# Performance work log

Hardware: AMD Instinct MI355X
Metric: run time of the kernel (lower is better)

## Reference

```python
import jax, jax.numpy as jnp
import numpy as np

D_MODEL = 512
D_K = 64
D_V = 64
N_HEADS = 8
N = 4096
EPS = 1e-5


def setup_inputs() -> dict:
    key = jax.random.key(0)
    ks = jax.random.split(key, 12)
    s = 1.0 / np.sqrt(D_MODEL)
    return {
        "Q": jax.random.normal(ks[0], (N, D_MODEL), dtype=jnp.float32),
        "K": jax.random.normal(ks[1], (N, D_MODEL), dtype=jnp.float32),
        "V": jax.random.normal(ks[2], (N, D_MODEL), dtype=jnp.float32),
        "W_Q": jax.random.normal(ks[3], (D_K * N_HEADS, D_MODEL), dtype=jnp.float32) * s,
        "b_Q": jnp.zeros((D_K * N_HEADS,), jnp.float32),
        "W_K": jax.random.normal(ks[4], (D_K * N_HEADS, D_MODEL), dtype=jnp.float32) * s,
        "b_K": jnp.zeros((D_K * N_HEADS,), jnp.float32),
        "W_V": jax.random.normal(ks[5], (D_V * N_HEADS, D_MODEL), dtype=jnp.float32) * s,
        "b_V": jnp.zeros((D_V * N_HEADS,), jnp.float32),
        "W_O": jax.random.normal(ks[6], (D_MODEL, N_HEADS * D_V), dtype=jnp.float32) * s,
        "b_O": jnp.zeros((D_MODEL,), jnp.float32),
        "gamma": jnp.ones((D_MODEL,), jnp.float32),
        "beta": jnp.zeros((D_MODEL,), jnp.float32),
    }


def reference(Q, K, V, W_Q, b_Q, W_K, b_K, W_V, b_V, W_O, b_O, gamma, beta):
    n = Q.shape[0]
    # projections (torch Linear: x @ W.T + b), then split heads: [N, H, dk]
    Qs = (Q @ W_Q.T + b_Q).reshape(n, N_HEADS, D_K)
    Ks = (K @ W_K.T + b_K).reshape(n, N_HEADS, D_K)
    Vs = (V @ W_V.T + b_V).reshape(n, N_HEADS, D_V)
    # per-head scaled dot-product attention over the N dim, batched via einsum
    scores = jnp.einsum("nhd,mhd->hnm", Qs, Ks) / np.sqrt(D_K)  # [H, N, N]
    attn = jax.nn.softmax(scores, axis=-1)
    ctx = jnp.einsum("hnm,mhd->nhd", attn, Vs)  # [N, H, dv]
    context = ctx.reshape(n, N_HEADS * D_V)  # concat heads (matches torch.cat order)
    out = context @ W_O.T + b_O + Q  # output proj + residual
    # LayerNorm over last dim
    mu = jnp.mean(out, axis=-1, keepdims=True)
    var = jnp.mean((out - mu) ** 2, axis=-1, keepdims=True)
    return (out - mu) * jax.lax.rsqrt(var + EPS) * gamma + beta
```

## Files before the change

### kernel.cpp

```cpp
#include <hip/hip_runtime.h>
#include <cstdint>

#define N_TOK 4096
#define DMODEL 512
#define NHEADS 8
#define HDIM 64

typedef unsigned short u16;
typedef __bf16 bf16x8 __attribute__((ext_vector_type(8)));
typedef float f32x4 __attribute__((ext_vector_type(4)));

union U128 { uint4 u; bf16x8 b; u16 s[8]; };

__device__ __forceinline__ u16 f2bf(float f) {
  uint32_t u = __builtin_bit_cast(uint32_t, f);
  u += 0x7FFFu + ((u >> 16) & 1u);
  return (u16)(u >> 16);
}
__device__ __forceinline__ float bf2f(u16 s) {
  uint32_t u = ((uint32_t)s) << 16;
  return __builtin_bit_cast(float, u);
}
__device__ __forceinline__ uint32_t fbit(float f) { return __builtin_bit_cast(uint32_t, f); }

#if __has_builtin(__builtin_amdgcn_exp2f)
#define EXP2(x) __builtin_amdgcn_exp2f(x)
#else
#define EXP2(x) __expf((x) * 0.6931471805599453f)
#endif

__device__ __forceinline__ void ldg2lds16(const void* g, void* s) {
  __builtin_amdgcn_global_load_lds(
      (const __attribute__((address_space(1))) void*)g,
      (__attribute__((address_space(3))) void*)s, 16, 0, 0);
}

__global__ __launch_bounds__(256) void cvt7_kernel(
    const float* __restrict__ Q, const float* __restrict__ K, const float* __restrict__ V,
    const float* __restrict__ WQ, const float* __restrict__ WK, const float* __restrict__ WV,
    const float* __restrict__ WO,
    u16* __restrict__ Qb, u16* __restrict__ Kb, u16* __restrict__ Vb,
    u16* __restrict__ WQb, u16* __restrict__ WKb, u16* __restrict__ WVb,
    u16* __restrict__ WOb)
{
  int b = blockIdx.x;
  const float* src; u16* dst; int rel;
  if      (b < 2048) { src = Q;  dst = Qb;  rel = b; }
  else if (b < 4096) { src = K;  dst = Kb;  rel = b - 2048; }
  else if (b < 6144) { src = V;  dst = Vb;  rel = b - 4096; }
  else if (b < 6400) { src = WQ; dst = WQb; rel = b - 6144; }
  else if (b < 6656) { src = WK; dst = WKb; rel = b - 6400; }
  else if (b < 6912) { src = WV; dst = WVb; rel = b - 6656; }
  else               { src = WO; dst = WOb; rel = b - 6912; }
  int i = (rel * 256 + threadIdx.x) * 4;
  float4 f = *(const float4*)(src + i);
  ushort4 o;
  o.x = f2bf(f.x); o.y = f2bf(f.y); o.z = f2bf(f.z); o.w = f2bf(f.w);
  *(ushort4*)(dst + i) = o;
}

__global__ __launch_bounds__(256) void proj3_kernel(
    const u16* __restrict__ Qb, const u16* __restrict__ Kb, const u16* __restrict__ Vb,
    const u16* __restrict__ WQb, const u16* __restrict__ WKb, const u16* __restrict__ WVb,
    const float* __restrict__ bQ, const float* __restrict__ bK, const float* __restrict__ bV,
    u16* __restrict__ Qs, u16* __restrict__ Ks, u16* __restrict__ Vt)
{
  const int z = blockIdx.z;
  const u16* A      = (z == 0) ? Qb : (z == 1) ? Kb : Vb;
  const u16* W      = (z == 0) ? WQb : (z == 1) ? WKb : WVb;
  const float* bias = (z == 0) ? bQ : (z == 1) ? bK : bV;

  const int m0 = blockIdx.x * 128;
  const int j0 = blockIdx.y * 64;
  const int tid = threadIdx.x;
  const int w = tid >> 6, lane = tid & 63, quad = lane >> 4, l = lane & 15;

  __shared__ bf16x8 sA[2][8][128];
  __shared__ bf16x8 sB[2][8][64];

  const f32x4 zero = {0.f, 0.f, 0.f, 0.f};
  f32x4 acc[2][4];
#pragma unroll
  for (int m = 0; m < 2; ++m)
#pragma unroll
    for (int s = 0; s < 4; ++s) acc[m][s] = zero;

  auto stage = [&](int kt, int buf) {
    const int k0 = kt * 64;
#pragma unroll
    for (int i = 0; i < 4; ++i) {
      const int chunk = 2 * w + (i >> 1), half = (i & 1) * 64;
      const u16* ag = A + (size_t)(m0 + half + lane) * DMODEL + k0 + chunk * 8;
      ldg2lds16(ag, (char*)&sA[buf][chunk][half]);
    }
#pragma unroll
    for (int i = 0; i < 2; ++i) {
      const int chunk = 2 * w + i;
      const u16* bg = W + (size_t)(j0 + lane) * DMODEL + k0 + chunk * 8;
      ldg2lds16(bg, (char*)&sB[buf][chunk][0]);
    }
  };

  stage(0, 0);
  __syncthreads();
  for (int kt = 0; kt < 8; ++kt) {
    const int buf = kt & 1;
    if (kt + 1 < 8) stage(kt + 1, buf ^ 1);
#pragma unroll
    for (int c = 0; c < 2; ++c) {
      bf16x8 af0 = sA[buf][c * 4 + quad][w * 32 + l];
      bf16x8 af1 = sA[buf][c * 4 + quad][w * 32 + 16 + l];
#pragma unroll
      for (int s = 0; s < 4; ++s) {
        bf16x8 bfb = sB[buf][c * 4 + quad][s * 16 + l];
        acc[0][s] = __builtin_amdgcn_mfma_f32_16x16x32_bf16(af0, bfb, acc[0][s], 0, 0, 0);
        acc[1][s] = __builtin_amdgcn_mfma_f32_16x16x32_bf16(af1, bfb, acc[1][s], 0, 0, 0);
      }
    }
    __syncthreads();
  }

#pragma unroll
  for (int m = 0; m < 2; ++m)
#pragma unroll
    for (int s = 0; s < 4; ++s) {
      int j = j0 + s * 16 + l;
      float bv = bias[j];
      int n0 = m0 + w * 32 + m * 16 + quad * 4;
      if (z < 2) {
        u16* Y = (z == 0) ? Qs : Ks;
#pragma unroll
        for (int r = 0; r < 4; ++r)
          Y[(size_t)(n0 + r) * DMODEL + j] = f2bf(acc[m][s][r] + bv);
      } else {
        ushort4 pk;
        pk.x = f2bf(acc[m][s][0] + bv); pk.y = f2bf(acc[m][s][1] + bv);
        pk.z = f2bf(acc[m][s][2] + bv); pk.w = f2bf(acc[m][s][3] + bv);
        *(ushort4*)(Vt + (size_t)j * N_TOK + n0) = pk;
      }
    }
}

__global__ __launch_bounds__(512, 4) void attn_kernel(
    const u16* __restrict__ Qs, const u16* __restrict__ Ks,
    const u16* __restrict__ Vt, u16* __restrict__ Opart, float* __restrict__ Lpart)
{
  const int hs = blockIdx.x;
  const int h = hs & 7, split = hs >> 3;
  const int qt = blockIdx.y;
  const int tid = threadIdx.x;
  const int w = tid >> 6, lane = tid & 63, quad = lane >> 4, l = lane & 15;

  __shared__ bf16x8 kch[2][8][64];
  __shared__ bf16x8 vch[2][8][64];
  __shared__ __align__(16) u16 pbuf[8][32][40];

  const int wq0 = qt * 256 + w * 32;

  bf16x8 qf[2][2];
#pragma unroll
  for (int c = 0; c < 2; ++c)
#pragma unroll
    for (int m = 0; m < 2; ++m) {
      U128 u;
      u.u = *(const uint4*)(Qs + (size_t)(wq0 + m * 16 + l) * DMODEL + h * HDIM + c * 32 + quad * 8);
#pragma unroll
      for (int j = 0; j < 8; ++j) u.s[j] = f2bf(bf2f(u.s[j]) * 0.18033688f);
      qf[c][m] = u.b;
    }

  const f32x4 zero = {0.f, 0.f, 0.f, 0.f};
  f32x4 o[2][4];
  float lsum[2] = {0.f, 0.f};
#pragma unroll
  for (int m = 0; m < 2; ++m)
#pragma unroll
    for (int s = 0; s < 4; ++s) o[m][s] = zero;

  auto stage = [&](int it, int buf) {
    const int j0 = split * 1024 + it * 64;
    if (w < 4) {
      const u16* kg = Ks + (size_t)(j0 + lane) * DMODEL + h * HDIM + w * 16;
      ldg2lds16(kg,     (char*)&kch[buf][2 * w][0]);
      ldg2lds16(kg + 8, (char*)&kch[buf][2 * w + 1][0]);
    } else {
      const int w2 = w - 4;
      const u16* vg = Vt + (size_t)(h * HDIM + lane) * N_TOK + j0 + w2 * 16;
      ldg2lds16(vg,     (char*)&vch[buf][2 * w2][0]);
      ldg2lds16(vg + 8, (char*)&vch[buf][2 * w2 + 1][0]);
    }
  };

  stage(0, 0);
  __syncthreads();

  for (int it = 0; it < 16; ++it) {
    const int buf = it & 1;
    if (it + 1 < 16) stage(it + 1, buf ^ 1);

#pragma unroll
    for (int kh = 0; kh < 2; ++kh) {
#pragma unroll
      for (int tt = 0; tt < 2; ++tt) {
        const int t = kh * 2 + tt;
        f32x4 sacc[2];
        sacc[0] = zero; sacc[1] = zero;
#pragma unroll
        for (int c = 0; c < 2; ++c) {
          bf16x8 kf = kch[buf][c * 4 + quad][t * 16 + l];
          sacc[0] = __builtin_amdgcn_mfma_f32_16x16x32_bf16(kf, qf[c][0], sacc[0], 0, 0, 0);
          sacc[1] = __builtin_amdgcn_mfma_f32_16x16x32_bf16(kf, qf[c][1], sacc[1], 0, 0, 0);
        }
#pragma unroll
        for (int m = 0; m < 2; ++m) {
          float p0 = EXP2(sacc[m][0]);
          float p1 = EXP2(sacc[m][1]);
          float p2 = EXP2(sacc[m][2]);
          float p3 = EXP2(sacc[m][3]);
          lsum[m] += (p0 + p1) + (p2 + p3);
          uint2 st;
          st.x = (fbit(p0) >> 16) | (fbit(p1) & 0xFFFF0000u);
          st.y = (fbit(p2) >> 16) | (fbit(p3) & 0xFFFF0000u);
          *(uint2*)&pbuf[w][m * 16 + l][tt * 16 + quad * 4] = st;
        }
      }
      U128 pf0, pf1;
      pf0.u = *(const uint4*)&pbuf[w][l][quad * 8];
      pf1.u = *(const uint4*)&pbuf[w][16 + l][quad * 8];
#pragma unroll
      for (int s = 0; s < 4; ++s) {
        bf16x8 vf = vch[buf][kh * 4 + quad][s * 16 + l];
        o[0][s] = __builtin_amdgcn_mfma_f32_16x16x32_bf16(pf0.b, vf, o[0][s], 0, 0, 0);
        o[1][s] = __builtin_amdgcn_mfma_f32_16x16x32_bf16(pf1.b, vf, o[1][s], 0, 0, 0);
      }
    }
    __syncthreads();
  }

#pragma unroll
  for (int m = 0; m < 2; ++m) {
    lsum[m] += __shfl_xor(lsum[m], 16);
    lsum[m] += __shfl_xor(lsum[m], 32);
  }
  if (quad == 0) {
    Lpart[((size_t)split * NHEADS + h) * N_TOK + wq0 + l]      = lsum[0];
    Lpart[((size_t)split * NHEADS + h) * N_TOK + wq0 + 16 + l] = lsum[1];
  }
  u16* Ob = Opart + ((size_t)(split * NHEADS + h) * N_TOK + wq0) * 64;
#pragma unroll
  for (int m = 0; m < 2; ++m)
#pragma unroll
    for (int s = 0; s < 4; ++s)
#pragma unroll
      for (int r = 0; r < 4; ++r)
        Ob[(size_t)(m * 16 + quad * 4 + r) * 64 + s * 16 + l] = f2bf(o[m][s][r]);
}

__global__ __launch_bounds__(256) void combine_kernel(
    const u16* __restrict__ Opart, const float* __restrict__ Lpart,
    u16* __restrict__ ctx)
{
  int idx = blockIdx.x * 256 + threadIdx.x;
  int n = idx >> 6;
  int c8 = idx & 63;
  int h = c8 >> 3;
  int vd0 = (c8 & 7) * 8;

  float acc[8] = {0, 0, 0, 0, 0, 0, 0, 0};
  float lsum = 0.f;
#pragma unroll
  for (int s = 0; s < 4; ++s) {
    U128 u;
    u.u = *(const uint4*)(Opart + ((size_t)(s * NHEADS + h) * N_TOK + n) * 64 + vd0);
#pragma unroll
    for (int j = 0; j < 8; ++j) acc[j] += bf2f(u.s[j]);
    lsum += Lpart[((size_t)s * NHEADS + h) * N_TOK + n];
  }
  float inv = 1.f / lsum;
  U128 u;
#pragma unroll
  for (int j = 0; j < 8; ++j) u.s[j] = f2bf(acc[j] * inv);
  *(uint4*)(ctx + (size_t)n * DMODEL + h * HDIM + vd0) = u.u;
}

__global__ __launch_bounds__(256) void gemmo_kernel(
    const u16* __restrict__ ctx, const u16* __restrict__ WOb,
    const float* __restrict__ bO, const float* __restrict__ resid,
    float* __restrict__ Y)
{
  const int m0 = blockIdx.x * 128;
  const int j0 = blockIdx.y * 64;
  const int tid = threadIdx.x;
  const int w = tid >> 6, lane = tid & 63, quad = lane >> 4, l = lane & 15;

  __shared__ bf16x8 sA[2][8][128];
  __shared__ bf16x8 sB[2][8][64];

  const f32x4 zero = {0.f, 0.f, 0.f, 0.f};
  f32x4 acc[2][4];
#pragma unroll
  for (int m = 0; m < 2; ++m)
#pragma unroll
    for (int s = 0; s < 4; ++s) acc[m][s] = zero;

  auto stage = [&](int kt, int buf) {
    const int k0 = kt * 64;
#pragma unroll
    for (int i = 0; i < 4; ++i) {
      const int chunk = 2 * w + (i >> 1), half = (i & 1) * 64;
      const u16* ag = ctx + (size_t)(m0 + half + lane) * DMODEL + k0 + chunk * 8;
      ldg2lds16(ag, (char*)&sA[buf][chunk][half]);
    }
#pragma unroll
    for (int i = 0; i < 2; ++i) {
      const int chunk = 2 * w + i;
      const u16* bg = WOb + (size_t)(j0 + lane) * DMODEL + k0 + chunk * 8;
      ldg2lds16(bg, (char*)&sB[buf][chunk][0]);
    }
  };

  stage(0, 0);
  __syncthreads();
  for (int kt = 0; kt < 8; ++kt) {
    const int buf = kt & 1;
    if (kt + 1 < 8) stage(kt + 1, buf ^ 1);
#pragma unroll
    for (int c = 0; c < 2; ++c) {
      bf16x8 af0 = sA[buf][c * 4 + quad][w * 32 + l];
      bf16x8 af1 = sA[buf][c * 4 + quad][w * 32 + 16 + l];
#pragma unroll
      for (int s = 0; s < 4; ++s) {
        bf16x8 bfb = sB[buf][c * 4 + quad][s * 16 + l];
        acc[0][s] = __builtin_amdgcn_mfma_f32_16x16x32_bf16(af0, bfb, acc[0][s], 0, 0, 0);
        acc[1][s] = __builtin_amdgcn_mfma_f32_16x16x32_bf16(af1, bfb, acc[1][s], 0, 0, 0);
      }
    }
    __syncthreads();
  }
#pragma unroll
  for (int m = 0; m < 2; ++m)
#pragma unroll
    for (int s = 0; s < 4; ++s) {
      int j = j0 + s * 16 + l;
      float bv = bO[j];
      int n0 = m0 + w * 32 + m * 16 + quad * 4;
#pragma unroll
      for (int r = 0; r < 4; ++r)
        Y[(size_t)(n0 + r) * DMODEL + j] = acc[m][s][r] + bv + resid[(size_t)(n0 + r) * DMODEL + j];
    }
}

__global__ __launch_bounds__(256) void ln_kernel(
    const float* __restrict__ X, const float* __restrict__ gamma,
    const float* __restrict__ beta, float* __restrict__ Y)
{
  const int w = threadIdx.x >> 6, lane = threadIdx.x & 63;
  const int row = blockIdx.x * 4 + w;
  const float* x = X + (size_t)row * DMODEL + lane * 8;
  float4 a = *(const float4*)x;
  float4 b = *(const float4*)(x + 4);

  float s = a.x + a.y + a.z + a.w + b.x + b.y + b.z + b.w;
#pragma unroll
  for (int m = 1; m < 64; m <<= 1) s += __shfl_xor(s, m);
  float mu = s * (1.f / DMODEL);

  float d0 = a.x - mu, d1 = a.y - mu, d2 = a.z - mu, d3 = a.w - mu;
  float d4 = b.x - mu, d5 = b.y - mu, d6 = b.z - mu, d7 = b.w - mu;
  float v = d0*d0 + d1*d1 + d2*d2 + d3*d3 + d4*d4 + d5*d5 + d6*d6 + d7*d7;
#pragma unroll
  for (int m = 1; m < 64; m <<= 1) v += __shfl_xor(v, m);
  float sc = rsqrtf(v * (1.f / DMODEL) + 1e-5f);

  const float* g = gamma + lane * 8;
  const float* be = beta + lane * 8;
  float4 go = *(const float4*)g;
  float4 g1 = *(const float4*)(g + 4);
  float4 bo = *(const float4*)be;
  float4 b1 = *(const float4*)(be + 4);

  float4 y0, y1;
  y0.x = d0 * sc * go.x + bo.x;  y0.y = d1 * sc * go.y + bo.y;
  y0.z = d2 * sc * go.z + bo.z;  y0.w = d3 * sc * go.w + bo.w;
  y1.x = d4 * sc * g1.x + b1.x;  y1.y = d5 * sc * g1.y + b1.y;
  y1.z = d6 * sc * g1.z + b1.z;  y1.w = d7 * sc * g1.w + b1.w;

  float* yp = Y + (size_t)row * DMODEL + lane * 8;
  *(float4*)yp = y0;
  *(float4*)(yp + 4) = y1;
}

extern "C" void kernel_launch(void* const* d_in, const int* in_sizes, int n_in,
                              void* d_out, int out_size, void* d_ws, size_t ws_size,
                              hipStream_t stream)
{
  const float* Q     = (const float*)d_in[0];
  const float* K     = (const float*)d_in[1];
  const float* V     = (const float*)d_in[2];
  const float* WQ    = (const float*)d_in[3];
  const float* bQ    = (const float*)d_in[4];
  const float* WK    = (const float*)d_in[5];
  const float* bK    = (const float*)d_in[6];
  const float* WV    = (const float*)d_in[7];
  const float* bV    = (const float*)d_in[8];
  const float* WO    = (const float*)d_in[9];
  const float* bO    = (const float*)d_in[10];
  const float* gamma = (const float*)d_in[11];
  const float* beta  = (const float*)d_in[12];

  const size_t MB = 1ull << 20;
  char* ws = (char*)d_ws;
  u16* Qb   = (u16*)(ws + 0 * MB);
  u16* Kb   = (u16*)(ws + 4 * MB);
  u16* Vb   = (u16*)(ws + 8 * MB);
  u16* WQb  = (u16*)(ws + 12 * MB);
  u16* WKb  = (u16*)(ws + 12 * MB + 512 * 1024);
  u16* WVb  = (u16*)(ws + 13 * MB);
  u16* WOb  = (u16*)(ws + 13 * MB + 512 * 1024);
  u16* Qs   = (u16*)(ws + 14 * MB);
  u16* Ks   = (u16*)(ws + 18 * MB);
  u16* Vt   = (u16*)(ws + 22 * MB);
  u16* ctx  = (u16*)(ws + 26 * MB);
  u16* Opart = (u16*)(ws + 30 * MB);
  float* tmp = (float*)(ws + 30 * MB);
  float* Lpart = (float*)(ws + 46 * MB);
  float* out = (float*)d_out;

  cvt7_kernel<<<7168, 256, 0, stream>>>(Q, K, V, WQ, WK, WV, WO,
                                        Qb, Kb, Vb, WQb, WKb, WVb, WOb);
  proj3_kernel<<<dim3(32, 8, 3), 256, 0, stream>>>(Qb, Kb, Vb, WQb, WKb, WVb,
                                                   bQ, bK, bV, Qs, Ks, Vt);
  attn_kernel<<<dim3(32, 16), 512, 0, stream>>>(Qs, Ks, Vt, Opart, Lpart);
  combine_kernel<<<1024, 256, 0, stream>>>(Opart, Lpart, ctx);
  gemmo_kernel<<<dim3(32, 8), 256, 0, stream>>>(ctx, WOb, bO, Q, tmp);
  ln_kernel<<<1024, 256, 0, stream>>>(tmp, gamma, beta, out);
}
```

Before: 182.3 us.

## Widen attention per-wave query tile, double KV splits, shrink output-proj tile

The attention kernel now uses 4 waves per block, each holding 64 query rows instead of 32. Each K/V tile staged in LDS is therefore reused across more MFMAs per wave. The key range is split 8 ways instead of 4, so the grid doubles, and the combine kernel reduces over 8 partials. The output-projection GEMM tile is halved to 64 rows so more blocks launch. The trade-off is higher register pressure per attention wave and twice the partial-output traffic in the combine step.

```diff
diff --git a/kernel.cpp b/kernel.cpp
--- a/kernel.cpp
+++ b/kernel.cpp
@@ -141,7 +141,7 @@
     }
 }
 
-__global__ __launch_bounds__(512, 4) void attn_kernel(
+__global__ __launch_bounds__(256, 3) void attn_kernel(
     const u16* __restrict__ Qs, const u16* __restrict__ Ks,
     const u16* __restrict__ Vt, u16* __restrict__ Opart, float* __restrict__ Lpart)
 {
@@ -153,15 +153,15 @@
 
   __shared__ bf16x8 kch[2][8][64];
   __shared__ bf16x8 vch[2][8][64];
-  __shared__ __align__(16) u16 pbuf[8][32][40];
-
-  const int wq0 = qt * 256 + w * 32;
-
-  bf16x8 qf[2][2];
+  __shared__ __align__(16) u16 pbuf[4][64][40];
+
+  const int wq0 = qt * 256 + w * 64;
+
+  bf16x8 qf[2][4];
 #pragma unroll
   for (int c = 0; c < 2; ++c)
 #pragma unroll
-    for (int m = 0; m < 2; ++m) {
+    for (int m = 0; m < 4; ++m) {
       U128 u;
       u.u = *(const uint4*)(Qs + (size_t)(wq0 + m * 16 + l) * DMODEL + h * HDIM + c * 32 + quad * 8);
 #pragma unroll
@@ -170,49 +170,57 @@
     }
 
   const f32x4 zero = {0.f, 0.f, 0.f, 0.f};
-  f32x4 o[2][4];
-  float lsum[2] = {0.f, 0.f};
-#pragma unroll
-  for (int m = 0; m < 2; ++m)
+  f32x4 o[4][4];
+  float lsum[4] = {0.f, 0.f, 0.f, 0.f};
+#pragma unroll
+  for (int m = 0; m < 4; ++m)
 #pragma unroll
     for (int s = 0; s < 4; ++s) o[m][s] = zero;
 
   auto stage = [&](int it, int buf) {
-    const int j0 = split * 1024 + it * 64;
-    if (w < 4) {
-      const u16* kg = Ks + (size_t)(j0 + lane) * DMODEL + h * HDIM + w * 16;
-      ldg2lds16(kg,     (char*)&kch[buf][2 * w][0]);
-      ldg2lds16(kg + 8, (char*)&kch[buf][2 * w + 1][0]);
+    const int j0 = split * 512 + it * 64;
+    if (w < 2) {
+#pragma unroll
+      for (int i = 0; i < 4; ++i) {
+        const int chunk = w * 4 + i;
+        const u16* kg = Ks + (size_t)(j0 + lane) * DMODEL + h * HDIM + chunk * 8;
+        ldg2lds16(kg, (char*)&kch[buf][chunk][0]);
+      }
     } else {
-      const int w2 = w - 4;
-      const u16* vg = Vt + (size_t)(h * HDIM + lane) * N_TOK + j0 + w2 * 16;
-      ldg2lds16(vg,     (char*)&vch[buf][2 * w2][0]);
-      ldg2lds16(vg + 8, (char*)&vch[buf][2 * w2 + 1][0]);
+#pragma unroll
+      for (int i = 0; i < 4; ++i) {
+        const int chunk = (w - 2) * 4 + i;
+        const u16* vg = Vt + (size_t)(h * HDIM + lane) * N_TOK + j0 + chunk * 8;
+        ldg2lds16(vg, (char*)&vch[buf][chunk][0]);
+      }
     }
   };
 
   stage(0, 0);
   __syncthreads();
 
-  for (int it = 0; it < 16; ++it) {
+  for (int it = 0; it < 8; ++it) {
     const int buf = it & 1;
-    if (it + 1 < 16) stage(it + 1, buf ^ 1);
+    if (it + 1 < 8) stage(it + 1, buf ^ 1);
 
 #pragma unroll
     for (int kh = 0; kh < 2; ++kh) {
 #pragma unroll
       for (int tt = 0; tt < 2; ++tt) {
         const int t = kh * 2 + tt;
-        f32x4 sacc[2];
-        sacc[0] = zero; sacc[1] = zero;
+        f32x4 sacc[4];
+#pragma unroll
+        for (int m = 0; m < 4; ++m) sacc[m] = zero;
 #pragma unroll
         for (int c = 0; c < 2; ++c) {
           bf16x8 kf = kch[buf][c * 4 + quad][t * 16 + l];
           sacc[0] = __builtin_amdgcn_mfma_f32_16x16x32_bf16(kf, qf[c][0], sacc[0], 0, 0, 0);
           sacc[1] = __builtin_amdgcn_mfma_f32_16x16x32_bf16(kf, qf[c][1], sacc[1], 0, 0, 0);
+          sacc[2] = __builtin_amdgcn_mfma_f32_16x16x32_bf16(kf, qf[c][2], sacc[2], 0, 0, 0);
+          sacc[3] = __builtin_amdgcn_mfma_f32_16x16x32_bf16(kf, qf[c][3], sacc[3], 0, 0, 0);
         }
 #pragma unroll
-        for (int m = 0; m < 2; ++m) {
+        for (int m = 0; m < 4; ++m) {
           float p0 = EXP2(sacc[m][0]);
           float p1 = EXP2(sacc[m][1]);
           float p2 = EXP2(sacc[m][2]);
@@ -224,31 +232,35 @@
           *(uint2*)&pbuf[w][m * 16 + l][tt * 16 + quad * 4] = st;
         }
       }
-      U128 pf0, pf1;
-      pf0.u = *(const uint4*)&pbuf[w][l][quad * 8];
-      pf1.u = *(const uint4*)&pbuf[w][16 + l][quad * 8];
+      U128 pf[4];
+#pragma unroll
+      for (int m = 0; m < 4; ++m)
+        pf[m].u = *(const uint4*)&pbuf[w][m * 16 + l][quad * 8];
 #pragma unroll
       for (int s = 0; s < 4; ++s) {
         bf16x8 vf = vch[buf][kh * 4 + quad][s * 16 + l];
-        o[0][s] = __builtin_amdgcn_mfma_f32_16x16x32_bf16(pf0.b, vf, o[0][s], 0, 0, 0);
-        o[1][s] = __builtin_amdgcn_mfma_f32_16x16x32_bf16(pf1.b, vf, o[1][s], 0, 0, 0);
+        o[0][s] = __builtin_amdgcn_mfma_f32_16x16x32_bf16(pf[0].b, vf, o[0][s], 0, 0, 0);
+        o[1][s] = __builtin_amdgcn_mfma_f32_16x16x32_bf16(pf[1].b, vf, o[1][s], 0, 0, 0);
+        o[2][s] = __builtin_amdgcn_mfma_f32_16x16x32_bf16(pf[2].b, vf, o[2][s], 0, 0, 0);
+        o[3][s] = __builtin_amdgcn_mfma_f32_16x16x32_bf16(pf[3].b, vf, o[3][s], 0, 0, 0);
       }
     }
     __syncthreads();
   }
 
 #pragma unroll
-  for (int m = 0; m < 2; ++m) {
+  for (int m = 0; m < 4; ++m) {
     lsum[m] += __shfl_xor(lsum[m], 16);
     lsum[m] += __shfl_xor(lsum[m], 32);
   }
   if (quad == 0) {
-    Lpart[((size_t)split * NHEADS + h) * N_TOK + wq0 + l]      = lsum[0];
-    Lpart[((size_t)split * NHEADS + h) * N_TOK + wq0 + 16 + l] = lsum[1];
+#pragma unroll
+    for (int m = 0; m < 4; ++m)
+      Lpart[((size_t)split * NHEADS + h) * N_TOK + wq0 + m * 16 + l] = lsum[m];
   }
   u16* Ob = Opart + ((size_t)(split * NHEADS + h) * N_TOK + wq0) * 64;
 #pragma unroll
-  for (int m = 0; m < 2; ++m)
+  for (int m = 0; m < 4; ++m)
 #pragma unroll
     for (int s = 0; s < 4; ++s)
 #pragma unroll
@@ -269,7 +281,7 @@
   float acc[8] = {0, 0, 0, 0, 0, 0, 0, 0};
   float lsum = 0.f;
 #pragma unroll
-  for (int s = 0; s < 4; ++s) {
+  for (int s = 0; s < 8; ++s) {
     U128 u;
     u.u = *(const uint4*)(Opart + ((size_t)(s * NHEADS + h) * N_TOK + n) * 64 + vd0);
 #pragma unroll
@@ -288,32 +300,26 @@
     const float* __restrict__ bO, const float* __restrict__ resid,
     float* __restrict__ Y)
 {
-  const int m0 = blockIdx.x * 128;
+  const int m0 = blockIdx.x * 64;
   const int j0 = blockIdx.y * 64;
   const int tid = threadIdx.x;
   const int w = tid >> 6, lane = tid & 63, quad = lane >> 4, l = lane & 15;
 
-  __shared__ bf16x8 sA[2][8][128];
+  __shared__ bf16x8 sA[2][8][64];
   __shared__ bf16x8 sB[2][8][64];
 
   const f32x4 zero = {0.f, 0.f, 0.f, 0.f};
-  f32x4 acc[2][4];
-#pragma unroll
-  for (int m = 0; m < 2; ++m)
-#pragma unroll
-    for (int s = 0; s < 4; ++s) acc[m][s] = zero;
+  f32x4 acc[4];
+#pragma unroll
+  for (int s = 0; s < 4; ++s) acc[s] = zero;
 
   auto stage = [&](int kt, int buf) {
     const int k0 = kt * 64;
 #pragma unroll
-    for (int i = 0; i < 4; ++i) {
-      const int chunk = 2 * w + (i >> 1), half = (i & 1) * 64;
-      const u16* ag = ctx + (size_t)(m0 + half + lane) * DMODEL + k0 + chunk * 8;
-      ldg2lds16(ag, (char*)&sA[buf][chunk][half]);
-    }
-#pragma unroll
     for (int i = 0; i < 2; ++i) {
       const int chunk = 2 * w + i;
+      const u16* ag = ctx + (size_t)(m0 + lane) * DMODEL + k0 + chunk * 8;
+      ldg2lds16(ag, (char*)&sA[buf][chunk][0]);
       const u16* bg = WOb + (size_t)(j0 + lane) * DMODEL + k0 + chunk * 8;
       ldg2lds16(bg, (char*)&sB[buf][chunk][0]);
     }
@@ -326,28 +332,24 @@
     if (kt + 1 < 8) stage(kt + 1, buf ^ 1);
 #pragma unroll
     for (int c = 0; c < 2; ++c) {
-      bf16x8 af0 = sA[buf][c * 4 + quad][w * 32 + l];
-      bf16x8 af1 = sA[buf][c * 4 + quad][w * 32 + 16 + l];
+      bf16x8 af = sA[buf][c * 4 + quad][w * 16 + l];
 #pragma unroll
       for (int s = 0; s < 4; ++s) {
         bf16x8 bfb = sB[buf][c * 4 + quad][s * 16 + l];
-        acc[0][s] = __builtin_amdgcn_mfma_f32_16x16x32_bf16(af0, bfb, acc[0][s], 0, 0, 0);
-        acc[1][s] = __builtin_amdgcn_mfma_f32_16x16x32_bf16(af1, bfb, acc[1][s], 0, 0, 0);
+        acc[s] = __builtin_amdgcn_mfma_f32_16x16x32_bf16(af, bfb, acc[s], 0, 0, 0);
       }
     }
     __syncthreads();
   }
 #pragma unroll
-  for (int m = 0; m < 2; ++m)
-#pragma unroll
-    for (int s = 0; s < 4; ++s) {
-      int j = j0 + s * 16 + l;
-      float bv = bO[j];
-      int n0 = m0 + w * 32 + m * 16 + quad * 4;
-#pragma unroll
-      for (int r = 0; r < 4; ++r)
-        Y[(size_t)(n0 + r) * DMODEL + j] = acc[m][s][r] + bv + resid[(size_t)(n0 + r) * DMODEL + j];
-    }
+  for (int s = 0; s < 4; ++s) {
+    int j = j0 + s * 16 + l;
+    float bv = bO[j];
+    int n0 = m0 + w * 16 + quad * 4;
+#pragma unroll
+    for (int r = 0; r < 4; ++r)
+      Y[(size_t)(n0 + r) * DMODEL + j] = acc[s][r] + bv + resid[(size_t)(n0 + r) * DMODEL + j];
+  }
 }
 
 __global__ __launch_bounds__(256) void ln_kernel(
@@ -423,15 +425,15 @@
   u16* ctx  = (u16*)(ws + 26 * MB);
   u16* Opart = (u16*)(ws + 30 * MB);
   float* tmp = (float*)(ws + 30 * MB);
-  float* Lpart = (float*)(ws + 46 * MB);
+  float* Lpart = (float*)(ws + 62 * MB);
   float* out = (float*)d_out;
 
   cvt7_kernel<<<7168, 256, 0, stream>>>(Q, K, V, WQ, WK, WV, WO,
                                         Qb, Kb, Vb, WQb, WKb, WVb, WOb);
   proj3_kernel<<<dim3(32, 8, 3), 256, 0, stream>>>(Qb, Kb, Vb, WQb, WKb, WVb,
                                                    bQ, bK, bV, Qs, Ks, Vt);
-  attn_kernel<<<dim3(32, 16), 512, 0, stream>>>(Qs, Ks, Vt, Opart, Lpart);
+  attn_kernel<<<dim3(64, 16), 256, 0, stream>>>(Qs, Ks, Vt, Opart, Lpart);
   combine_kernel<<<1024, 256, 0, stream>>>(Opart, Lpart, ctx);
-  gemmo_kernel<<<dim3(32, 8), 256, 0, stream>>>(ctx, WOb, bO, Q, tmp);
+  gemmo_kernel<<<dim3(64, 8), 256, 0, stream>>>(ctx, WOb, bO, Q, tmp);
   ln_kernel<<<1024, 256, 0, stream>>>(tmp, gamma, beta, out);
 }
```

Result: slower. 277.1 us (+52.0%).

## Fuse all stages into one persistent kernel with atomic grid barriers

Applied to the files above, without the earlier changes.

Replaces the six separate launches (convert, QKV projection, attention, split combine, output GEMM, LayerNorm) with one persistent 512-block kernel. The stages are separated by software grid barriers built on a global atomic counter. The aim is to remove per-launch overhead and the drain/fill gaps between launches. In exchange, the projection and output GEMMs are re-tiled to smaller 64x64 tiles per block. The design also relies on all 512 blocks being co-resident, and it adds barrier spin cost plus a memset per call.

```diff
diff --git a/kernel.cpp b/kernel.cpp
--- a/kernel.cpp
+++ b/kernel.cpp
@@ -35,359 +35,341 @@
       (__attribute__((address_space(3))) void*)s, 16, 0, 0);
 }
 
-__global__ __launch_bounds__(256) void cvt7_kernel(
+__device__ __forceinline__ void gridbar(unsigned int* cnt, unsigned int target) {
+  __syncthreads();
+  if (threadIdx.x == 0) {
+    __threadfence();
+    __hip_atomic_fetch_add(cnt, 1u, __ATOMIC_RELEASE, __HIP_MEMORY_SCOPE_AGENT);
+    while (__hip_atomic_load(cnt, __ATOMIC_ACQUIRE, __HIP_MEMORY_SCOPE_AGENT) < target)
+      __builtin_amdgcn_s_sleep(4);
+    __threadfence();
+  }
+  __syncthreads();
+}
+
+__global__ __launch_bounds__(512, 4) void fused_kernel(
     const float* __restrict__ Q, const float* __restrict__ K, const float* __restrict__ V,
-    const float* __restrict__ WQ, const float* __restrict__ WK, const float* __restrict__ WV,
-    const float* __restrict__ WO,
+    const float* __restrict__ WQ, const float* __restrict__ bQ,
+    const float* __restrict__ WK, const float* __restrict__ bK,
+    const float* __restrict__ WV, const float* __restrict__ bV,
+    const float* __restrict__ WO, const float* __restrict__ bO,
+    const float* __restrict__ gamma, const float* __restrict__ beta,
     u16* __restrict__ Qb, u16* __restrict__ Kb, u16* __restrict__ Vb,
     u16* __restrict__ WQb, u16* __restrict__ WKb, u16* __restrict__ WVb,
-    u16* __restrict__ WOb)
+    u16* __restrict__ WOb,
+    u16* __restrict__ Qs, u16* __restrict__ Ks, u16* __restrict__ Vt,
+    u16* __restrict__ ctx, u16* __restrict__ Opart, float* __restrict__ tmp,
+    float* __restrict__ Lpart, float* __restrict__ out,
+    unsigned int* __restrict__ cnt)
 {
-  int b = blockIdx.x;
-  const float* src; u16* dst; int rel;
-  if      (b < 2048) { src = Q;  dst = Qb;  rel = b; }
-  else if (b < 4096) { src = K;  dst = Kb;  rel = b - 2048; }
-  else if (b < 6144) { src = V;  dst = Vb;  rel = b - 4096; }
-  else if (b < 6400) { src = WQ; dst = WQb; rel = b - 6144; }
-  else if (b < 6656) { src = WK; dst = WKb; rel = b - 6400; }
-  else if (b < 6912) { src = WV; dst = WVb; rel = b - 6656; }
-  else               { src = WO; dst = WOb; rel = b - 6912; }
-  int i = (rel * 256 + threadIdx.x) * 4;
-  float4 f = *(const float4*)(src + i);
-  ushort4 o;
-  o.x = f2bf(f.x); o.y = f2bf(f.y); o.z = f2bf(f.z); o.w = f2bf(f.w);
-  *(ushort4*)(dst + i) = o;
-}
-
-__global__ __launch_bounds__(256) void proj3_kernel(
-    const u16* __restrict__ Qb, const u16* __restrict__ Kb, const u16* __restrict__ Vb,
-    const u16* __restrict__ WQb, const u16* __restrict__ WKb, const u16* __restrict__ WVb,
-    const float* __restrict__ bQ, const float* __restrict__ bK, const float* __restrict__ bV,
-    u16* __restrict__ Qs, u16* __restrict__ Ks, u16* __restrict__ Vt)
-{
-  const int z = blockIdx.z;
-  const u16* A      = (z == 0) ? Qb : (z == 1) ? Kb : Vb;
-  const u16* W      = (z == 0) ? WQb : (z == 1) ? WKb : WVb;
-  const float* bias = (z == 0) ? bQ : (z == 1) ? bK : bV;
-
-  const int m0 = blockIdx.x * 128;
-  const int j0 = blockIdx.y * 64;
+  __shared__ __align__(16) char smem[53248];
+
   const int tid = threadIdx.x;
+  const int bid = blockIdx.x;
   const int w = tid >> 6, lane = tid & 63, quad = lane >> 4, l = lane & 15;
-
-  __shared__ bf16x8 sA[2][8][128];
-  __shared__ bf16x8 sB[2][8][64];
-
   const f32x4 zero = {0.f, 0.f, 0.f, 0.f};
-  f32x4 acc[2][4];
-#pragma unroll
-  for (int m = 0; m < 2; ++m)
-#pragma unroll
-    for (int s = 0; s < 4; ++s) acc[m][s] = zero;
-
-  auto stage = [&](int kt, int buf) {
-    const int k0 = kt * 64;
-#pragma unroll
-    for (int i = 0; i < 4; ++i) {
-      const int chunk = 2 * w + (i >> 1), half = (i & 1) * 64;
-      const u16* ag = A + (size_t)(m0 + half + lane) * DMODEL + k0 + chunk * 8;
-      ldg2lds16(ag, (char*)&sA[buf][chunk][half]);
-    }
-#pragma unroll
-    for (int i = 0; i < 2; ++i) {
-      const int chunk = 2 * w + i;
-      const u16* bg = W + (size_t)(j0 + lane) * DMODEL + k0 + chunk * 8;
-      ldg2lds16(bg, (char*)&sB[buf][chunk][0]);
-    }
-  };
-
-  stage(0, 0);
-  __syncthreads();
-  for (int kt = 0; kt < 8; ++kt) {
-    const int buf = kt & 1;
-    if (kt + 1 < 8) stage(kt + 1, buf ^ 1);
-#pragma unroll
-    for (int c = 0; c < 2; ++c) {
-      bf16x8 af0 = sA[buf][c * 4 + quad][w * 32 + l];
-      bf16x8 af1 = sA[buf][c * 4 + quad][w * 32 + 16 + l];
-#pragma unroll
-      for (int s = 0; s < 4; ++s) {
-        bf16x8 bfb = sB[buf][c * 4 + quad][s * 16 + l];
-        acc[0][s] = __builtin_amdgcn_mfma_f32_16x16x32_bf16(af0, bfb, acc[0][s], 0, 0, 0);
-        acc[1][s] = __builtin_amdgcn_mfma_f32_16x16x32_bf16(af1, bfb, acc[1][s], 0, 0, 0);
-      }
-    }
+
+  {
+    const int gtid = bid * 512 + tid;
+#pragma unroll
+    for (int a = 0; a < 3; ++a) {
+      const float* s = (a == 0) ? Q : (a == 1) ? K : V;
+      u16* d = (a == 0) ? Qb : (a == 1) ? Kb : Vb;
+#pragma unroll
+      for (int rep = 0; rep < 2; ++rep) {
+        int i = (gtid + rep * 262144) * 4;
+        float4 f = *(const float4*)(s + i);
+        ushort4 o4;
+        o4.x = f2bf(f.x); o4.y = f2bf(f.y); o4.z = f2bf(f.z); o4.w = f2bf(f.w);
+        *(ushort4*)(d + i) = o4;
+      }
+    }
+    if (gtid < 65536) {
+      int i = gtid * 4;
+#pragma unroll
+      for (int a = 0; a < 4; ++a) {
+        const float* s = (a == 0) ? WQ : (a == 1) ? WK : (a == 2) ? WV : WO;
+        u16* d = (a == 0) ? WQb : (a == 1) ? WKb : (a == 2) ? WVb : WOb;
+        float4 f = *(const float4*)(s + i);
+        ushort4 o4;
+        o4.x = f2bf(f.x); o4.y = f2bf(f.y); o4.z = f2bf(f.z); o4.w = f2bf(f.w);
+        *(ushort4*)(d + i) = o4;
+      }
+    }
+  }
+  gridbar(cnt, 512);
+
+  {
+    bf16x8 (*sA)[8][64] = (bf16x8(*)[8][64])smem;
+    bf16x8 (*sB)[8][64] = (bf16x8(*)[8][64])(smem + 16384);
+    const int wr = w & 3;
+    const int ws_ = w >> 2;
+
+#pragma unroll
+    for (int z = 0; z < 3; ++z) {
+      const int m0 = (bid >> 3) * 64, j0 = (bid & 7) * 64;
+      const u16* A      = (z == 0) ? Qb : (z == 1) ? Kb : Vb;
+      const u16* W      = (z == 0) ? WQb : (z == 1) ? WKb : WVb;
+      const float* bias = (z == 0) ? bQ : (z == 1) ? bK : bV;
+
+      f32x4 acc[2];
+      acc[0] = zero; acc[1] = zero;
+
+      auto stage = [&](int kt, int buf) {
+        const int k0 = kt * 64;
+        ldg2lds16(A + (size_t)(m0 + lane) * DMODEL + k0 + w * 8, (char*)&sA[buf][w][0]);
+        ldg2lds16(W + (size_t)(j0 + lane) * DMODEL + k0 + w * 8, (char*)&sB[buf][w][0]);
+      };
+
+      stage(0, 0);
+      __syncthreads();
+      for (int kt = 0; kt < 8; ++kt) {
+        const int buf = kt & 1;
+        if (kt + 1 < 8) stage(kt + 1, buf ^ 1);
+#pragma unroll
+        for (int c = 0; c < 2; ++c) {
+          bf16x8 af = sA[buf][c * 4 + quad][wr * 16 + l];
+#pragma unroll
+          for (int s = 0; s < 2; ++s) {
+            bf16x8 bfb = sB[buf][c * 4 + quad][(ws_ * 2 + s) * 16 + l];
+            acc[s] = __builtin_amdgcn_mfma_f32_16x16x32_bf16(af, bfb, acc[s], 0, 0, 0);
+          }
+        }
+        __syncthreads();
+      }
+#pragma unroll
+      for (int s = 0; s < 2; ++s) {
+        int j = j0 + (ws_ * 2 + s) * 16 + l;
+        float bv = bias[j];
+        int n0 = m0 + wr * 16 + quad * 4;
+        if (z < 2) {
+          u16* Y = (z == 0) ? Qs : Ks;
+#pragma unroll
+          for (int r = 0; r < 4; ++r)
+            Y[(size_t)(n0 + r) * DMODEL + j] = f2bf(acc[s][r] + bv);
+        } else {
+          ushort4 pk;
+          pk.x = f2bf(acc[s][0] + bv); pk.y = f2bf(acc[s][1] + bv);
+          pk.z = f2bf(acc[s][2] + bv); pk.w = f2bf(acc[s][3] + bv);
+          *(ushort4*)(Vt + (size_t)j * N_TOK + n0) = pk;
+        }
+      }
+      __syncthreads();
+    }
+  }
+  gridbar(cnt, 1024);
+
+  {
+    const int h = bid & 7, split = (bid >> 3) & 3, qt = bid >> 5;
+    bf16x8 (*kch)[8][64] = (bf16x8(*)[8][64])smem;
+    bf16x8 (*vch)[8][64] = (bf16x8(*)[8][64])(smem + 16384);
+    u16 (*pbuf)[32][40] = (u16(*)[32][40])(smem + 32768);
+
+    const int wq0 = qt * 256 + w * 32;
+
+    bf16x8 qf[2][2];
+#pragma unroll
+    for (int c = 0; c < 2; ++c)
+#pragma unroll
+      for (int m = 0; m < 2; ++m) {
+        U128 u;
+        u.u = *(const uint4*)(Qs + (size_t)(wq0 + m * 16 + l) * DMODEL + h * HDIM + c * 32 + quad * 8);
+#pragma unroll
+        for (int j = 0; j < 8; ++j) u.s[j] = f2bf(bf2f(u.s[j]) * 0.18033688f);
+        qf[c][m] = u.b;
+      }
+
+    f32x4 o[2][4];
+    float lsum[2] = {0.f, 0.f};
+#pragma unroll
+    for (int m = 0; m < 2; ++m)
+#pragma unroll
+      for (int s = 0; s < 4; ++s) o[m][s] = zero;
+
+    auto stage = [&](int it, int buf) {
+      const int j0 = split * 1024 + it * 64;
+      if (w < 4) {
+        const u16* kg = Ks + (size_t)(j0 + lane) * DMODEL + h * HDIM + w * 16;
+        ldg2lds16(kg,     (char*)&kch[buf][2 * w][0]);
+        ldg2lds16(kg + 8, (char*)&kch[buf][2 * w + 1][0]);
+      } else {
+        const int w2 = w - 4;
+        const u16* vg = Vt + (size_t)(h * HDIM + lane) * N_TOK + j0 + w2 * 16;
+        ldg2lds16(vg,     (char*)&vch[buf][2 * w2][0]);
+        ldg2lds16(vg + 8, (char*)&vch[buf][2 * w2 + 1][0]);
+      }
+    };
+
+    stage(0, 0);
     __syncthreads();
-  }
-
-#pragma unroll
-  for (int m = 0; m < 2; ++m)
+
+    for (int it = 0; it < 16; ++it) {
+      const int buf = it & 1;
+      if (it + 1 < 16) stage(it + 1, buf ^ 1);
+
+#pragma unroll
+      for (int kh = 0; kh < 2; ++kh) {
+#pragma unroll
+        for (int tt = 0; tt < 2; ++tt) {
+          const int t = kh * 2 + tt;
+          f32x4 sacc[2];
+          sacc[0] = zero; sacc[1] = zero;
+#pragma unroll
+          for (int c = 0; c < 2; ++c) {
+            bf16x8 kf = kch[buf][c * 4 + quad][t * 16 + l];
+            sacc[0] = __builtin_amdgcn_mfma_f32_16x16x32_bf16(kf, qf[c][0], sacc[0], 0, 0, 0);
+            sacc[1] = __builtin_amdgcn_mfma_f32_16x16x32_bf16(kf, qf[c][1], sacc[1], 0, 0, 0);
+          }
+#pragma unroll
+          for (int m = 0; m < 2; ++m) {
+            float p0 = EXP2(sacc[m][0]);
+            float p1 = EXP2(sacc[m][1]);
+            float p2 = EXP2(sacc[m][2]);
+            float p3 = EXP2(sacc[m][3]);
+            lsum[m] += (p0 + p1) + (p2 + p3);
+            uint2 st;
+            st.x = (fbit(p0) >> 16) | (fbit(p1) & 0xFFFF0000u);
+            st.y = (fbit(p2) >> 16) | (fbit(p3) & 0xFFFF0000u);
+            *(uint2*)&pbuf[w][m * 16 + l][tt * 16 + quad * 4] = st;
+          }
+        }
+        U128 pf0, pf1;
+        pf0.u = *(const uint4*)&pbuf[w][l][quad * 8];
+        pf1.u = *(const uint4*)&pbuf[w][16 + l][quad * 8];
+#pragma unroll
+        for (int s = 0; s < 4; ++s) {
+          bf16x8 vf = vch[buf][kh * 4 + quad][s * 16 + l];
+          o[0][s] = __builtin_amdgcn_mfma_f32_16x16x32_bf16(pf0.b, vf, o[0][s], 0, 0, 0);
+          o[1][s] = __builtin_amdgcn_mfma_f32_16x16x32_bf16(pf1.b, vf, o[1][s], 0, 0, 0);
+        }
+      }
+      __syncthreads();
+    }
+
+#pragma unroll
+    for (int m = 0; m < 2; ++m) {
+      lsum[m] += __shfl_xor(lsum[m], 16);
+      lsum[m] += __shfl_xor(lsum[m], 32);
+    }
+    if (quad == 0) {
+      Lpart[((size_t)split * NHEADS + h) * N_TOK + wq0 + l]      = lsum[0];
+      Lpart[((size_t)split * NHEADS + h) * N_TOK + wq0 + 16 + l] = lsum[1];
+    }
+    u16* Ob = Opart + ((size_t)(split * NHEADS + h) * N_TOK + wq0) * 64;
+#pragma unroll
+    for (int m = 0; m < 2; ++m)
+#pragma unroll
+      for (int s = 0; s < 4; ++s)
+#pragma unroll
+        for (int r = 0; r < 4; ++r)
+          Ob[(size_t)(m * 16 + quad * 4 + r) * 64 + s * 16 + l] = f2bf(o[m][s][r]);
+  }
+  gridbar(cnt, 1536);
+
+  {
+    int idx = bid * 512 + tid;
+    int n = idx >> 6;
+    int c8 = idx & 63;
+    int h = c8 >> 3;
+    int vd0 = (c8 & 7) * 8;
+
+    float acc[8] = {0, 0, 0, 0, 0, 0, 0, 0};
+    float lsum = 0.f;
 #pragma unroll
     for (int s = 0; s < 4; ++s) {
-      int j = j0 + s * 16 + l;
-      float bv = bias[j];
-      int n0 = m0 + w * 32 + m * 16 + quad * 4;
-      if (z < 2) {
-        u16* Y = (z == 0) ? Qs : Ks;
-#pragma unroll
-        for (int r = 0; r < 4; ++r)
-          Y[(size_t)(n0 + r) * DMODEL + j] = f2bf(acc[m][s][r] + bv);
-      } else {
-        ushort4 pk;
-        pk.x = f2bf(acc[m][s][0] + bv); pk.y = f2bf(acc[m][s][1] + bv);
-        pk.z = f2bf(acc[m][s][2] + bv); pk.w = f2bf(acc[m][s][3] + bv);
-        *(ushort4*)(Vt + (size_t)j * N_TOK + n0) = pk;
-      }
-    }
-}
-
-__global__ __launch_bounds__(512, 4) void attn_kernel(
-    const u16* __restrict__ Qs, const u16* __restrict__ Ks,
-    const u16* __restrict__ Vt, u16* __restrict__ Opart, float* __restrict__ Lpart)
-{
-  const int hs = blockIdx.x;
-  const int h = hs & 7, split = hs >> 3;
-  const int qt = blockIdx.y;
-  const int tid = threadIdx.x;
-  const int w = tid >> 6, lane = tid & 63, quad = lane >> 4, l = lane & 15;
-
-  __shared__ bf16x8 kch[2][8][64];
-  __shared__ bf16x8 vch[2][8][64];
-  __shared__ __align__(16) u16 pbuf[8][32][40];
-
-  const int wq0 = qt * 256 + w * 32;
-
-  bf16x8 qf[2][2];
-#pragma unroll
-  for (int c = 0; c < 2; ++c)
-#pragma unroll
-    for (int m = 0; m < 2; ++m) {
       U128 u;
-      u.u = *(const uint4*)(Qs + (size_t)(wq0 + m * 16 + l) * DMODEL + h * HDIM + c * 32 + quad * 8);
-#pragma unroll
-      for (int j = 0; j < 8; ++j) u.s[j] = f2bf(bf2f(u.s[j]) * 0.18033688f);
-      qf[c][m] = u.b;
-    }
-
-  const f32x4 zero = {0.f, 0.f, 0.f, 0.f};
-  f32x4 o[2][4];
-  float lsum[2] = {0.f, 0.f};
-#pragma unroll
-  for (int m = 0; m < 2; ++m)
-#pragma unroll
-    for (int s = 0; s < 4; ++s) o[m][s] = zero;
-
-  auto stage = [&](int it, int buf) {
-    const int j0 = split * 1024 + it * 64;
-    if (w < 4) {
-      const u16* kg = Ks + (size_t)(j0 + lane) * DMODEL + h * HDIM + w * 16;
-      ldg2lds16(kg,     (char*)&kch[buf][2 * w][0]);
-      ldg2lds16(kg + 8, (char*)&kch[buf][2 * w + 1][0]);
-    } else {
-      const int w2 = w - 4;
-      const u16* vg = Vt + (size_t)(h * HDIM + lane) * N_TOK + j0 + w2 * 16;
-      ldg2lds16(vg,     (char*)&vch[buf][2 * w2][0]);
-      ldg2lds16(vg + 8, (char*)&vch[buf][2 * w2 + 1][0]);
-    }
-  };
-
-  stage(0, 0);
-  __syncthreads();
-
-  for (int it = 0; it < 16; ++it) {
-    const int buf = it & 1;
-    if (it + 1 < 16) stage(it + 1, buf ^ 1);
-
-#pragma unroll
-    for (int kh = 0; kh < 2; ++kh) {
-#pragma unroll
-      for (int tt = 0; tt < 2; ++tt) {
-        const int t = kh * 2 + tt;
-        f32x4 sacc[2];
-        sacc[0] = zero; sacc[1] = zero;
-#pragma unroll
-        for (int c = 0; c < 2; ++c) {
-          bf16x8 kf = kch[buf][c * 4 + quad][t * 16 + l];
-          sacc[0] = __builtin_amdgcn_mfma_f32_16x16x32_bf16(kf, qf[c][0], sacc[0], 0, 0, 0);
-          sacc[1] = __builtin_amdgcn_mfma_f32_16x16x32_bf16(kf, qf[c][1], sacc[1], 0, 0, 0);
+      u.u = *(const uint4*)(Opart + ((size_t)(s * NHEADS + h) * N_TOK + n) * 64 + vd0);
+#pragma unroll
+      for (int j = 0; j < 8; ++j) acc[j] += bf2f(u.s[j]);
+      lsum += Lpart[((size_t)s * NHEADS + h) * N_TOK + n];
+    }
+    float inv = 1.f / lsum;
+    U128 u;
+#pragma unroll
+    for (int j = 0; j < 8; ++j) u.s[j] = f2bf(acc[j] * inv);
+    *(uint4*)(ctx + (size_t)n * DMODEL + h * HDIM + vd0) = u.u;
+  }
+  gridbar(cnt, 2048);
+
+  {
+    bf16x8 (*sA)[8][64] = (bf16x8(*)[8][64])smem;
+    bf16x8 (*sB)[8][64] = (bf16x8(*)[8][64])(smem + 16384);
+    const int m0 = (bid >> 3) * 64, j0 = (bid & 7) * 64;
+    const int wr = w & 3;
+    const int ws_ = w >> 2;
+
+    f32x4 acc[2];
+    acc[0] = zero; acc[1] = zero;
+
+    auto stage = [&](int kt, int buf) {
+      const int k0 = kt * 64;
+      ldg2lds16(ctx + (size_t)(m0 + lane) * DMODEL + k0 + w * 8, (char*)&sA[buf][w][0]);
+      ldg2lds16(WOb + (size_t)(j0 + lane) * DMODEL + k0 + w * 8, (char*)&sB[buf][w][0]);
+    };
+
+    stage(0, 0);
+    __syncthreads();
+    for (int kt = 0; kt < 8; ++kt) {
+      const int buf = kt & 1;
+      if (kt + 1 < 8) stage(kt + 1, buf ^ 1);
+#pragma unroll
+      for (int c = 0; c < 2; ++c) {
+        bf16x8 af = sA[buf][c * 4 + quad][wr * 16 + l];
+#pragma unroll
+        for (int s = 0; s < 2; ++s) {
+          bf16x8 bfb = sB[buf][c * 4 + quad][(ws_ * 2 + s) * 16 + l];
+          acc[s] = __builtin_amdgcn_mfma_f32_16x16x32_bf16(af, bfb, acc[s], 0, 0, 0);
         }
-#pragma unroll
-        for (int m = 0; m < 2; ++m) {
-          float p0 = EXP2(sacc[m][0]);
-          float p1 = EXP2(sacc[m][1]);
-          float p2 = EXP2(sacc[m][2]);
-          float p3 = EXP2(sacc[m][3]);
-          lsum[m] += (p0 + p1) + (p2 + p3);
-          uint2 st;
-          st.x = (fbit(p0) >> 16) | (fbit(p1) & 0xFFFF0000u);
-          st.y = (fbit(p2) >> 16) | (fbit(p3) & 0xFFFF0000u);
-          *(uint2*)&pbuf[w][m * 16 + l][tt * 16 + quad * 4] = st;
-        }
-      }
-      U128 pf0, pf1;
-      pf0.u = *(const uint4*)&pbuf[w][l][quad * 8];
-      pf1.u = *(const uint4*)&pbuf[w][16 + l][quad * 8];
-#pragma unroll
-      for (int s = 0; s < 4; ++s) {
-        bf16x8 vf = vch[buf][kh * 4 + quad][s * 16 + l];
-        o[0][s] = __builtin_amdgcn_mfma_f32_16x16x32_bf16(pf0.b, vf, o[0][s], 0, 0, 0);
-        o[1][s] = __builtin_amdgcn_mfma_f32_16x16x32_bf16(pf1.b, vf, o[1][s], 0, 0, 0);
-      }
-    }
-    __syncthreads();
-  }
-
-#pragma unroll
-  for (int m = 0; m < 2; ++m) {
-    lsum[m] += __shfl_xor(lsum[m], 16);
-    lsum[m] += __shfl_xor(lsum[m], 32);
-  }
-  if (quad == 0) {
-    Lpart[((size_t)split * NHEADS + h) * N_TOK + wq0 + l]      = lsum[0];
-    Lpart[((size_t)split * NHEADS + h) * N_TOK + wq0 + 16 + l] = lsum[1];
-  }
-  u16* Ob = Opart + ((size_t)(split * NHEADS + h) * N_TOK + wq0) * 64;
-#pragma unroll
-  for (int m = 0; m < 2; ++m)
-#pragma unroll
-    for (int s = 0; s < 4; ++s)
+      }
+      __syncthreads();
+    }
+#pragma unroll
+    for (int s = 0; s < 2; ++s) {
+      int j = j0 + (ws_ * 2 + s) * 16 + l;
+      float bv = bO[j];
+      int n0 = m0 + wr * 16 + quad * 4;
 #pragma unroll
       for (int r = 0; r < 4; ++r)
-        Ob[(size_t)(m * 16 + quad * 4 + r) * 64 + s * 16 + l] = f2bf(o[m][s][r]);
-}
-
-__global__ __launch_bounds__(256) void combine_kernel(
-    const u16* __restrict__ Opart, const float* __restrict__ Lpart,
-    u16* __restrict__ ctx)
-{
-  int idx = blockIdx.x * 256 + threadIdx.x;
-  int n = idx >> 6;
-  int c8 = idx & 63;
-  int h = c8 >> 3;
-  int vd0 = (c8 & 7) * 8;
-
-  float acc[8] = {0, 0, 0, 0, 0, 0, 0, 0};
-  float lsum = 0.f;
-#pragma unroll
-  for (int s = 0; s < 4; ++s) {
-    U128 u;
-    u.u = *(const uint4*)(Opart + ((size_t)(s * NHEADS + h) * N_TOK + n) * 64 + vd0);
-#pragma unroll
-    for (int j = 0; j < 8; ++j) acc[j] += bf2f(u.s[j]);
-    lsum += Lpart[((size_t)s * NHEADS + h) * N_TOK + n];
-  }
-  float inv = 1.f / lsum;
-  U128 u;
-#pragma unroll
-  for (int j = 0; j < 8; ++j) u.s[j] = f2bf(acc[j] * inv);
-  *(uint4*)(ctx + (size_t)n * DMODEL + h * HDIM + vd0) = u.u;
-}
-
-__global__ __launch_bounds__(256) void gemmo_kernel(
-    const u16* __restrict__ ctx, const u16* __restrict__ WOb,
-    const float* __restrict__ bO, const float* __restrict__ resid,
-    float* __restrict__ Y)
-{
-  const int m0 = blockIdx.x * 128;
-  const int j0 = blockIdx.y * 64;
-  const int tid = threadIdx.x;
-  const int w = tid >> 6, lane = tid & 63, quad = lane >> 4, l = lane & 15;
-
-  __shared__ bf16x8 sA[2][8][128];
-  __shared__ bf16x8 sB[2][8][64];
-
-  const f32x4 zero = {0.f, 0.f, 0.f, 0.f};
-  f32x4 acc[2][4];
-#pragma unroll
-  for (int m = 0; m < 2; ++m)
-#pragma unroll
-    for (int s = 0; s < 4; ++s) acc[m][s] = zero;
-
-  auto stage = [&](int kt, int buf) {
-    const int k0 = kt * 64;
-#pragma unroll
-    for (int i = 0; i < 4; ++i) {
-      const int chunk = 2 * w + (i >> 1), half = (i & 1) * 64;
-      const u16* ag = ctx + (size_t)(m0 + half + lane) * DMODEL + k0 + chunk * 8;
-      ldg2lds16(ag, (char*)&sA[buf][chunk][half]);
-    }
-#pragma unroll
-    for (int i = 0; i < 2; ++i) {
-      const int chunk = 2 * w + i;
-      const u16* bg = WOb + (size_t)(j0 + lane) * DMODEL + k0 + chunk * 8;
-      ldg2lds16(bg, (char*)&sB[buf][chunk][0]);
-    }
-  };
-
-  stage(0, 0);
-  __syncthreads();
-  for (int kt = 0; kt < 8; ++kt) {
-    const int buf = kt & 1;
-    if (kt + 1 < 8) stage(kt + 1, buf ^ 1);
-#pragma unroll
-    for (int c = 0; c < 2; ++c) {
-      bf16x8 af0 = sA[buf][c * 4 + quad][w * 32 + l];
-      bf16x8 af1 = sA[buf][c * 4 + quad][w * 32 + 16 + l];
-#pragma unroll
-      for (int s = 0; s < 4; ++s) {
-        bf16x8 bfb = sB[buf][c * 4 + quad][s * 16 + l];
-        acc[0][s] = __builtin_amdgcn_mfma_f32_16x16x32_bf16(af0, bfb, acc[0][s], 0, 0, 0);
-        acc[1][s] = __builtin_amdgcn_mfma_f32_16x16x32_bf16(af1, bfb, acc[1][s], 0, 0, 0);
-      }
-    }
-    __syncthreads();
-  }
-#pragma unroll
-  for (int m = 0; m < 2; ++m)
-#pragma unroll
-    for (int s = 0; s < 4; ++s) {
-      int j = j0 + s * 16 + l;
-      float bv = bO[j];
-      int n0 = m0 + w * 32 + m * 16 + quad * 4;
-#pragma unroll
-      for (int r = 0; r < 4; ++r)
-        Y[(size_t)(n0 + r) * DMODEL + j] = acc[m][s][r] + bv + resid[(size_t)(n0 + r) * DMODEL + j];
-    }
-}
-
-__global__ __launch_bounds__(256) void ln_kernel(
-    const float* __restrict__ X, const float* __restrict__ gamma,
-    const float* __restrict__ beta, float* __restrict__ Y)
-{
-  const int w = threadIdx.x >> 6, lane = threadIdx.x & 63;
-  const int row = blockIdx.x * 4 + w;
-  const float* x = X + (size_t)row * DMODEL + lane * 8;
-  float4 a = *(const float4*)x;
-  float4 b = *(const float4*)(x + 4);
-
-  float s = a.x + a.y + a.z + a.w + b.x + b.y + b.z + b.w;
-#pragma unroll
-  for (int m = 1; m < 64; m <<= 1) s += __shfl_xor(s, m);
-  float mu = s * (1.f / DMODEL);
-
-  float d0 = a.x - mu, d1 = a.y - mu, d2 = a.z - mu, d3 = a.w - mu;
-  float d4 = b.x - mu, d5 = b.y - mu, d6 = b.z - mu, d7 = b.w - mu;
-  float v = d0*d0 + d1*d1 + d2*d2 + d3*d3 + d4*d4 + d5*d5 + d6*d6 + d7*d7;
-#pragma unroll
-  for (int m = 1; m < 64; m <<= 1) v += __shfl_xor(v, m);
-  float sc = rsqrtf(v * (1.f / DMODEL) + 1e-5f);
-
-  const float* g = gamma + lane * 8;
-  const float* be = beta + lane * 8;
-  float4 go = *(const float4*)g;
-  float4 g1 = *(const float4*)(g + 4);
-  float4 bo = *(const float4*)be;
-  float4 b1 = *(const float4*)(be + 4);
-
-  float4 y0, y1;
-  y0.x = d0 * sc * go.x + bo.x;  y0.y = d1 * sc * go.y + bo.y;
-  y0.z = d2 * sc * go.z + bo.z;  y0.w = d3 * sc * go.w + bo.w;
-  y1.x = d4 * sc * g1.x + b1.x;  y1.y = d5 * sc * g1.y + b1.y;
-  y1.z = d6 * sc * g1.z + b1.z;  y1.w = d7 * sc * g1.w + b1.w;
-
-  float* yp = Y + (size_t)row * DMODEL + lane * 8;
-  *(float4*)yp = y0;
-  *(float4*)(yp + 4) = y1;
+        tmp[(size_t)(n0 + r) * DMODEL + j] = acc[s][r] + bv + Q[(size_t)(n0 + r) * DMODEL + j];
+    }
+  }
+  gridbar(cnt, 2560);
+
+  {
+    const int row = bid * 8 + w;
+    const float* x = tmp + (size_t)row * DMODEL + lane * 8;
+    float4 a = *(const float4*)x;
+    float4 b = *(const float4*)(x + 4);
+
+    float s = a.x + a.y + a.z + a.w + b.x + b.y + b.z + b.w;
+#pragma unroll
+    for (int m = 1; m < 64; m <<= 1) s += __shfl_xor(s, m);
+    float mu = s * (1.f / DMODEL);
+
+    float d0 = a.x - mu, d1 = a.y - mu, d2 = a.z - mu, d3 = a.w - mu;
+    float d4 = b.x - mu, d5 = b.y - mu, d6 = b.z - mu, d7 = b.w - mu;
+    float v = d0*d0 + d1*d1 + d2*d2 + d3*d3 + d4*d4 + d5*d5 + d6*d6 + d7*d7;
+#pragma unroll
+    for (int m = 1; m < 64; m <<= 1) v += __shfl_xor(v, m);
+    float sc = rsqrtf(v * (1.f / DMODEL) + 1e-5f);
+
+    const float* g = gamma + lane * 8;
+    const float* be = beta + lane * 8;
+    float4 go = *(const float4*)g;
+    float4 g1 = *(const float4*)(g + 4);
+    float4 bo = *(const float4*)be;
+    float4 b1 = *(const float4*)(be + 4);
+
+    float4 y0, y1;
+    y0.x = d0 * sc * go.x + bo.x;  y0.y = d1 * sc * go.y + bo.y;
+    y0.z = d2 * sc * go.z + bo.z;  y0.w = d3 * sc * go.w + bo.w;
+    y1.x = d4 * sc * g1.x + b1.x;  y1.y = d5 * sc * g1.y + b1.y;
+    y1.z = d6 * sc * g1.z + b1.z;  y1.w = d7 * sc * g1.w + b1.w;
+
+    float* yp = out + (size_t)row * DMODEL + lane * 8;
+    *(float4*)yp = y0;
+    *(float4*)(yp + 4) = y1;
+  }
 }
 
 extern "C" void kernel_launch(void* const* d_in, const int* in_sizes, int n_in,
@@ -410,28 +392,26 @@
 
   const size_t MB = 1ull << 20;
   char* ws = (char*)d_ws;
-  u16* Qb   = (u16*)(ws + 0 * MB);
-  u16* Kb   = (u16*)(ws + 4 * MB);
-  u16* Vb   = (u16*)(ws + 8 * MB);
-  u16* WQb  = (u16*)(ws + 12 * MB);
-  u16* WKb  = (u16*)(ws + 12 * MB + 512 * 1024);
-  u16* WVb  = (u16*)(ws + 13 * MB);
-  u16* WOb  = (u16*)(ws + 13 * MB + 512 * 1024);
-  u16* Qs   = (u16*)(ws + 14 * MB);
-  u16* Ks   = (u16*)(ws + 18 * MB);
-  u16* Vt   = (u16*)(ws + 22 * MB);
-  u16* ctx  = (u16*)(ws + 26 * MB);
+  u16* Qb    = (u16*)(ws + 0 * MB);
+  u16* Kb    = (u16*)(ws + 4 * MB);
+  u16* Vb    = (u16*)(ws + 8 * MB);
+  u16* WQb   = (u16*)(ws + 12 * MB);
+  u16* WKb   = (u16*)(ws + 12 * MB + 512 * 1024);
+  u16* WVb   = (u16*)(ws + 13 * MB);
+  u16* WOb   = (u16*)(ws + 13 * MB + 512 * 1024);
+  u16* Qs    = (u16*)(ws + 14 * MB);
+  u16* Ks    = (u16*)(ws + 18 * MB);
+  u16* Vt    = (u16*)(ws + 22 * MB);
+  u16* ctxp  = (u16*)(ws + 26 * MB);
   u16* Opart = (u16*)(ws + 30 * MB);
   float* tmp = (float*)(ws + 30 * MB);
   float* Lpart = (float*)(ws + 46 * MB);
-  float* out = (float*)d_out;
-
-  cvt7_kernel<<<7168, 256, 0, stream>>>(Q, K, V, WQ, WK, WV, WO,
-                                        Qb, Kb, Vb, WQb, WKb, WVb, WOb);
-  proj3_kernel<<<dim3(32, 8, 3), 256, 0, stream>>>(Qb, Kb, Vb, WQb, WKb, WVb,
-                                                   bQ, bK, bV, Qs, Ks, Vt);
-  attn_kernel<<<dim3(32, 16), 512, 0, stream>>>(Qs, Ks, Vt, Opart, Lpart);
-  combine_kernel<<<1024, 256, 0, stream>>>(Opart, Lpart, ctx);
-  gemmo_kernel<<<dim3(32, 8), 256, 0, stream>>>(ctx, WOb, bO, Q, tmp);
-  ln_kernel<<<1024, 256, 0, stream>>>(tmp, gamma, beta, out);
-}
+  unsigned int* cnt = (unsigned int*)(ws + 47 * MB);
+  float* outp = (float*)d_out;
+
+  hipMemsetAsync(cnt, 0, 128, stream);
+  fused_kernel<<<512, 512, 0, stream>>>(
+      Q, K, V, WQ, bQ, WK, bK, WV, bV, WO, bO, gamma, beta,
+      Qb, Kb, Vb, WQb, WKb, WVb, WOb,
+      Qs, Ks, Vt, ctxp, Opart, tmp, Lpart, outp, cnt);
+}
```

After: 599.9 us. 229% more time.
